# Optimization experiments

Measured on AMD Instinct MI355X. Metric: run time of the kernel, lower is better.

The kernel has to match this reference:

```python
import jax, jax.numpy as jnp
import numpy as np

N, T, E, A, D, O, S, R = 64, 1000, 512, 256, 256, 80, 64, 2
ATT_RANGE = 10
H = 4 * D  # LSTM hidden size = 1024
K = 31     # location conv kernel width


def setup_inputs() -> dict:
    key = jax.random.key(0)
    ks = jax.random.split(key, 16)
    def rn(k, shape, scale=0.05):
        return (jax.random.normal(k, shape) * scale).astype(jnp.float32)
    return {
        "input_enc": jax.random.normal(ks[0], (N, T, E), jnp.float32),
        "input_dec": jax.random.normal(ks[1], (N, O), jnp.float32),
        "spkr_vec": jax.random.normal(ks[2], (N, 1, S), jnp.float32),
        "lengths_enc": jnp.full((N,), T, dtype=jnp.int32),
        "w_enc": rn(ks[3], (E, A)), "b_enc": jnp.zeros((A,), jnp.float32),
        "w_spkr": rn(ks[4], (S, A)),
        "conv_w": rn(ks[5], (A, 1, K)),
        "w_proj": rn(ks[6], (A, 1)), "b_proj": jnp.zeros((1,), jnp.float32),
        "w_p1": rn(ks[7], (O + S, 2 * D)), "b_p1": jnp.zeros((2 * D,), jnp.float32),
        "w_p2": rn(ks[8], (2 * D, D)), "b_p2": jnp.zeros((D,), jnp.float32),
        "w_ih0": rn(ks[9], (E + D + S, 4 * H)), "w_hh0": rn(ks[10], (H, 4 * H)),
        "b_ih0": jnp.zeros((4 * H,), jnp.float32), "b_hh0": jnp.zeros((4 * H,), jnp.float32),
        "w_ih1": rn(ks[11], (H, 4 * H)), "w_hh1": rn(ks[12], (H, 4 * H)),
        "b_ih1": jnp.zeros((4 * H,), jnp.float32), "b_hh1": jnp.zeros((4 * H,), jnp.float32),
        "w_out": rn(ks[13], (E + H, O * R)), "b_out": jnp.zeros((O * R,), jnp.float32),
    }


def _softsign(x):
    return x / (1.0 + jnp.abs(x))


def _lstm_cell_zero_state(x, w_ih, b_ih, b_hh):
    # h0 = c0 = 0, so the w_hh contribution vanishes on the first step
    gates = x @ w_ih + b_ih + b_hh          # [N, 4H]
    i, f, g, o = jnp.split(gates, 4, axis=-1)  # torch gate order i,f,g,o
    c = jax.nn.sigmoid(i) * jnp.tanh(g)
    return jax.nn.sigmoid(o) * jnp.tanh(c)


def reference(input_enc, input_dec, spkr_vec, lengths_enc,
              w_enc, b_enc, w_spkr, conv_w, w_proj, b_proj,
              w_p1, b_p1, w_p2, b_p2,
              w_ih0, w_hh0, b_ih0, b_hh0, w_ih1, w_hh1, b_ih1, b_hh1,
              w_out, b_out):
    n, t_enc, _ = input_enc.shape
    # initial attention weights: one-hot at t=0 (null_state branch)
    a0 = jnp.zeros((n, t_enc), input_enc.dtype).at[:, 0].set(1.0)

    bias_enc = _softsign(input_enc @ w_enc + b_enc)   # [N, T, A]
    bias_spkr = _softsign(spkr_vec @ w_spkr)          # [N, 1, A] broadcast

    # location features: conv1d over prev attention, padding 15, no bias
    prev_feat = jax.lax.conv_general_dilated(
        a0[:, None, :], conv_w, (1,), [(K // 2, K // 2)],
        dimension_numbers=("NCH", "OIH", "NCH"))    # [N, A, T]
    prev_feat = prev_feat.transpose(0, 2, 1)          # [N, T, A]

    # hidden is None on the first step -> in_att_dec = 0
    e = bias_enc + bias_spkr + prev_feat              # [N, T, A]

    # windowed attention mask around argmax of previous weights (no grad)
    max_idx = jnp.argmax(a0, axis=1)                  # [N]
    lim = jnp.maximum(lengths_enc.astype(jnp.int32) - 1, 0)  # [N]
    offs = jnp.arange(ATT_RANGE, dtype=jnp.int32)
    idx1 = jnp.minimum(jnp.maximum(max_idx[:, None] + offs, 0), lim[:, None])
    idx2 = jnp.minimum(jnp.maximum(max_idx[:, None] - offs, 0), lim[:, None])
    idxs = jnp.concatenate([idx1, idx2], axis=1)      # [N, 2*ATT_RANGE]
    rows = jnp.arange(n)[:, None]
    att_mask = jnp.zeros((n, t_enc), e.dtype).at[rows, idxs].set(1.0)
    att_mask = jax.lax.stop_gradient(att_mask)

    logit = (jnp.tanh(e) @ w_proj + b_proj)[..., 0]   # [N, T]
    logit = logit - jnp.max(logit, axis=1, keepdims=True)
    w = jnp.exp(logit) * att_mask
    att = w / jnp.maximum(jnp.sum(w, axis=1, keepdims=True), 1e-12)  # F.normalize p=1

    context = jnp.einsum("nt,nte->ne", att, input_enc)  # [N, E]

    # prenet (dropout in eval mode = identity)
    spkr = spkr_vec[:, 0, :]
    pre = jnp.concatenate([input_dec, spkr], axis=-1)
    pre = jax.nn.relu(pre @ w_p1 + b_p1)
    pre = jax.nn.relu(pre @ w_p2 + b_p2)               # [N, D]

    x = jnp.concatenate([pre, context, spkr], axis=-1)  # [N, D+E+S]
    h1 = _lstm_cell_zero_state(x, w_ih0, b_ih0, b_hh0)   # [N, H]
    h2 = _lstm_cell_zero_state(h1, w_ih1, b_ih1, b_hh1)  # [N, H]
    _ = (w_hh0, w_hh1)  # recurrent weights unused on first step (zero state)

    dec = jnp.concatenate([h2, context], axis=-1)        # [N, H+E]
    out = (dec @ w_out + b_out).reshape(n, R, O)         # [N, r_factor, O]
    return out
```

## Files before the change

kernel.cpp:

```cpp
#include <hip/hip_runtime.h>
#include <hip/hip_bf16.h>
#include <math.h>

#define N_   64
#define T_   1000
#define E_   512
#define A_   256
#define O_   80
#define S_   64
#define H_   1024
#define G4_  4096
#define KC_  31

__device__ __forceinline__ float sigmoidf_(float x) { return 1.f / (1.f + __expf(-x)); }
__device__ __forceinline__ float softsignf_(float x) { return x / (1.f + fabsf(x)); }

__global__ __launch_bounds__(512) void logits_kernel(
    const float* __restrict__ enc,
    const float* __restrict__ spkr,
    const float* __restrict__ w_enc,
    const float* __restrict__ b_enc,
    const float* __restrict__ w_spkr,
    const float* __restrict__ conv_w,
    const float* __restrict__ w_proj,
    float* __restrict__ part) {
  int n  = blockIdx.x;
  int aq = blockIdx.y;
  int tid = threadIdx.x;
  int al = tid & 63;
  int kw = tid >> 6;
  int a  = aq * 64 + al;

  __shared__ float smem[5120];
  __shared__ float sp[S_];
  __shared__ float bsl[S_];

  if (tid < S_) sp[tid] = spkr[n * S_ + tid];
  {
    const float4* src = (const float4*)(enc + (size_t)n * T_ * E_);
    float4* dst = (float4*)smem;
    for (int i = tid; i < 1280; i += 512) dst[i] = src[i];
  }
  __syncthreads();

  if (tid < S_) {
    float b = 0.f;
    #pragma unroll 8
    for (int s = 0; s < S_; ++s) b += sp[s] * w_spkr[s * A_ + aq * 64 + tid];
    bsl[tid] = softsignf_(b);
  }

  float acc[10];
  #pragma unroll
  for (int t = 0; t < 10; ++t) acc[t] = 0.f;
  const int kbase = kw * 64;
  const float* wcol = w_enc + a;
  #pragma unroll 8
  for (int k = 0; k < 64; ++k) {
    float we = wcol[(size_t)(kbase + k) * A_];
    #pragma unroll
    for (int t = 0; t < 10; ++t)
      acc[t] = fmaf(smem[t * E_ + kbase + k], we, acc[t]);
  }

  __syncthreads();
  #pragma unroll
  for (int t = 0; t < 10; ++t) smem[(kw * 10 + t) * 64 + al] = acc[t];
  __syncthreads();

  #pragma unroll
  for (int tb = 0; tb < 10; tb += 8) {
    int t = tb + kw;
    if (t < 10 && (tb == 0 || kw < 2)) {
      float p = b_enc[a];
      #pragma unroll
      for (int w = 0; w < 8; ++w) p += smem[(w * 10 + t) * 64 + al];
      float e = softsignf_(p) + bsl[al] + conv_w[a * KC_ + (15 - t)];
      float l = tanhf(e) * w_proj[a];
      #pragma unroll
      for (int off = 32; off > 0; off >>= 1) l += __shfl_down(l, off);
      if (al == 0) part[(n * 10 + t) * 4 + aq] = l;
    }
  }
}

__global__ __launch_bounds__(512) void ctx_prenet_kernel(
    const float* __restrict__ enc,
    const float* __restrict__ dec_in,
    const float* __restrict__ spkr,
    const int*   __restrict__ lengths,
    const float* __restrict__ part,
    const float* __restrict__ w_p1,
    const float* __restrict__ b_p1,
    const float* __restrict__ w_p2,
    const float* __restrict__ b_p2,
    float* __restrict__ xbuf) {
  int n = blockIdx.x;
  int tid = threadIdx.x;
  __shared__ float att[10];
  __shared__ float incat[O_ + S_];
  __shared__ float pre1[512];
  __shared__ float pp2[2][A_];

  if (tid < S_) {
    float s = spkr[n * S_ + tid];
    incat[O_ + tid] = s;
    xbuf[n * 832 + 768 + tid] = s;
  }
  if (tid < O_) incat[tid] = dec_in[n * O_ + tid];
  if (tid == 0) {
    int lim = lengths[n] - 1; if (lim < 0) lim = 0;
    int tmax = lim < 9 ? lim : 9;
    float lg[10];
    float m = -1e30f;
    for (int t = 0; t <= tmax; ++t) {
      const float* p = &part[(n * 10 + t) * 4];
      lg[t] = p[0] + p[1] + p[2] + p[3];
      m = fmaxf(m, lg[t]);
    }
    float ssum = 0.f;
    for (int t = 0; t <= tmax; ++t) { float w = __expf(lg[t] - m); att[t] = w; ssum += w; }
    float inv = 1.f / fmaxf(ssum, 1e-12f);
    for (int t = 0; t <= tmax; ++t) att[t] *= inv;
    for (int t = tmax + 1; t < 10; ++t) att[t] = 0.f;
  }
  __syncthreads();

  {
    float c = 0.f;
    #pragma unroll
    for (int t = 0; t < 10; ++t)
      c = fmaf(att[t], enc[(size_t)n * T_ * E_ + t * E_ + tid], c);
    xbuf[n * 832 + 256 + tid] = c;
  }

  {
    float v = b_p1[tid];
    #pragma unroll 8
    for (int k = 0; k < O_ + S_; ++k) v = fmaf(incat[k], w_p1[k * 512 + tid], v);
    pre1[tid] = fmaxf(v, 0.f);
  }
  __syncthreads();

  {
    int c  = tid & 255;
    int kh = tid >> 8;
    float v = 0.f;
    #pragma unroll 8
    for (int k = kh * 256; k < kh * 256 + 256; ++k)
      v = fmaf(pre1[k], w_p2[k * A_ + c], v);
    pp2[kh][c] = v;
  }
  __syncthreads();
  if (tid < A_) {
    float v = b_p2[tid] + pp2[0][tid] + pp2[1][tid];
    xbuf[n * 832 + tid] = fmaxf(v, 0.f);
  }
}

__global__ __launch_bounds__(512) void gemm_gates_kernel(
    const float* __restrict__ X, int ldx, int K,
    const float* __restrict__ W,
    const float* __restrict__ b1,
    const float* __restrict__ b2,
    float* __restrict__ G) {
  int bt = blockIdx.x;
  int c0 = bt * 16; if (c0 >= 1024) c0 += 1024;
  int tid = threadIdx.x;
  int kh  = tid >> 8;
  int lt  = tid & 255;
  int tr  = lt >> 4;
  int tc  = lt & 15;
  int c   = c0 + tc;
  int Kh  = K >> 1;
  int kbeg = kh * Kh;
  int NC  = Kh >> 5;

  int rr  = lt & 63;
  int kb8 = (lt >> 6) << 3;
  int wr  = lt >> 4;
  int wc  = lt & 15;

  __shared__ float xs[2][2][32][64];
  __shared__ float wsl[2][2][32][16];
  __shared__ float red[16][16][4];

  const float* xsrc = X + (size_t)rr * ldx + kbeg + kb8;
  const float* wsrc = W + (size_t)(kbeg + wr) * G4_ + c0 + wc;

  float4 xv0 = ((const float4*)xsrc)[0];
  float4 xv1 = ((const float4*)(xsrc + 4))[0];
  float  wv0 = wsrc[0];
  float  wv1 = wsrc[(size_t)16 * G4_];
  {
    float* d = &xs[kh][0][kb8][rr];
    d[0]   = xv0.x; d[64]  = xv0.y; d[128] = xv0.z; d[192] = xv0.w;
    d[256] = xv1.x; d[320] = xv1.y; d[384] = xv1.z; d[448] = xv1.w;
    wsl[kh][0][wr][wc]      = wv0;
    wsl[kh][0][wr + 16][wc] = wv1;
  }
  __syncthreads();

  float acc0 = 0.f, acc1 = 0.f, acc2 = 0.f, acc3 = 0.f;
  for (int ch = 0; ch < NC; ++ch) {
    int buf = ch & 1;
    bool more = (ch + 1 < NC);
    if (more) {
      const float* s = xsrc + (ch + 1) * 32;
      xv0 = ((const float4*)s)[0];
      xv1 = ((const float4*)(s + 4))[0];
      const float* wsp = wsrc + (size_t)(ch + 1) * 32 * G4_;
      wv0 = wsp[0];
      wv1 = wsp[(size_t)16 * G4_];
    }
    const float* xb = &xs[kh][buf][0][tr * 4];
    const float* wb = &wsl[kh][buf][0][tc];
    #pragma unroll
    for (int kk = 0; kk < 32; ++kk) {
      float w = wb[kk * 16];
      float4 xv = *(const float4*)(xb + kk * 64);
      acc0 = fmaf(xv.x, w, acc0);
      acc1 = fmaf(xv.y, w, acc1);
      acc2 = fmaf(xv.z, w, acc2);
      acc3 = fmaf(xv.w, w, acc3);
    }
    if (more) {
      float* d = &xs[kh][buf ^ 1][kb8][rr];
      d[0]   = xv0.x; d[64]  = xv0.y; d[128] = xv0.z; d[192] = xv0.w;
      d[256] = xv1.x; d[320] = xv1.y; d[384] = xv1.z; d[448] = xv1.w;
      wsl[kh][buf ^ 1][wr][wc]      = wv0;
      wsl[kh][buf ^ 1][wr + 16][wc] = wv1;
    }
    __syncthreads();
  }

  if (kh == 1) {
    red[tr][tc][0] = acc0; red[tr][tc][1] = acc1;
    red[tr][tc][2] = acc2; red[tr][tc][3] = acc3;
  }
  __syncthreads();
  if (kh == 0) {
    float bb = b1[c] + b2[c];
    int r = tr * 4;
    G[(size_t)(r + 0) * G4_ + c] = acc0 + red[tr][tc][0] + bb;
    G[(size_t)(r + 1) * G4_ + c] = acc1 + red[tr][tc][1] + bb;
    G[(size_t)(r + 2) * G4_ + c] = acc2 + red[tr][tc][2] + bb;
    G[(size_t)(r + 3) * G4_ + c] = acc3 + red[tr][tc][3] + bb;
  }
}

__global__ void lstm_act_kernel(const float* __restrict__ G, float* __restrict__ H) {
  int idx = blockIdx.x * 256 + threadIdx.x;
  int n = idx >> 10;
  int j = idx & 1023;
  float gi = G[(size_t)n * G4_ + j];
  float gg = G[(size_t)n * G4_ + 2048 + j];
  float go = G[(size_t)n * G4_ + 3072 + j];
  float cc = sigmoidf_(gi) * tanhf(gg);
  H[n * H_ + j] = sigmoidf_(go) * tanhf(cc);
}

#define DLP 1544
__global__ __launch_bounds__(512) void out_kernel(
    const float* __restrict__ gates,
    const float* __restrict__ xbuf,
    const float* __restrict__ w_out,
    const float* __restrict__ b_out,
    float* __restrict__ out) {
  int bn = blockIdx.x >> 3;
  int c0 = (blockIdx.x & 7) * 20;
  int tid = threadIdx.x;
  __shared__ float dl[8][DLP];
  __shared__ float pp[3][160];

  for (int idx = tid; idx < 8 * 1536; idx += 512) {
    int nl = idx / 1536;
    int k  = idx % 1536;
    int n  = bn * 8 + nl;
    if (k < 1024) {
      float gi = gates[(size_t)n * G4_ + k];
      float gg = gates[(size_t)n * G4_ + 2048 + k];
      float go = gates[(size_t)n * G4_ + 3072 + k];
      dl[nl][k] = sigmoidf_(go) * tanhf(sigmoidf_(gi) * tanhf(gg));
    } else {
      dl[nl][k] = xbuf[n * 832 + 256 + (k - 1024)];
    }
  }
  __syncthreads();

  if (tid < 480) {
    int kq = tid / 160;
    int o  = tid % 160;
    int nl = o / 20;
    int cl = o % 20;
    const float* wp = w_out + (size_t)(kq * 512) * 160 + c0 + cl;
    const float* dp = &dl[nl][kq * 512];
    float acc = 0.f;
    #pragma unroll 8
    for (int k = 0; k < 512; ++k) acc = fmaf(dp[k], wp[(size_t)k * 160], acc);
    pp[kq][o] = acc;
  }
  __syncthreads();
  if (tid < 160) {
    int nl = tid / 20;
    int cl = tid % 20;
    float v = b_out[c0 + cl] + pp[0][tid] + pp[1][tid] + pp[2][tid];
    out[(size_t)(bn * 8 + nl) * 160 + c0 + cl] = v;
  }
}

extern "C" void kernel_launch(void* const* d_in, const int* in_sizes, int n_in,
                              void* d_out, int out_size, void* d_ws, size_t ws_size,
                              hipStream_t stream) {
  const float* input_enc = (const float*)d_in[0];
  const float* input_dec = (const float*)d_in[1];
  const float* spkr_vec  = (const float*)d_in[2];
  const int*   lengths   = (const int*)  d_in[3];
  const float* w_enc     = (const float*)d_in[4];
  const float* b_enc     = (const float*)d_in[5];
  const float* w_spkr    = (const float*)d_in[6];
  const float* conv_w    = (const float*)d_in[7];
  const float* w_proj    = (const float*)d_in[8];
  const float* w_p1      = (const float*)d_in[10];
  const float* b_p1      = (const float*)d_in[11];
  const float* w_p2      = (const float*)d_in[12];
  const float* b_p2      = (const float*)d_in[13];
  const float* w_ih0     = (const float*)d_in[14];
  const float* b_ih0     = (const float*)d_in[16];
  const float* b_hh0     = (const float*)d_in[17];
  const float* w_ih1     = (const float*)d_in[18];
  const float* b_ih1     = (const float*)d_in[20];
  const float* b_hh1     = (const float*)d_in[21];
  const float* w_out     = (const float*)d_in[22];
  const float* b_out     = (const float*)d_in[23];

  float* ws    = (float*)d_ws;
  float* part  = ws;
  float* xbuf  = ws + 4096;
  float* gates = ws + 65536;
  float* h1    = ws + 327680;
  float* out   = (float*)d_out;

  hipLaunchKernelGGL(logits_kernel, dim3(64, 4), dim3(512), 0, stream,
                     input_enc, spkr_vec, w_enc, b_enc, w_spkr, conv_w, w_proj, part);
  hipLaunchKernelGGL(ctx_prenet_kernel, dim3(64), dim3(512), 0, stream,
                     input_enc, input_dec, spkr_vec, lengths, part,
                     w_p1, b_p1, w_p2, b_p2, xbuf);
  hipLaunchKernelGGL(gemm_gates_kernel, dim3(192), dim3(512), 0, stream,
                     xbuf, 832, 832, w_ih0, b_ih0, b_hh0, gates);
  hipLaunchKernelGGL(lstm_act_kernel, dim3(256), dim3(256), 0, stream, gates, h1);
  hipLaunchKernelGGL(gemm_gates_kernel, dim3(192), dim3(512), 0, stream,
                     h1, 1024, 1024, w_ih1, b_ih1, b_hh1, gates);
  hipLaunchKernelGGL(out_kernel, dim3(64), dim3(512), 0, stream,
                     gates, xbuf, w_out, b_out, out);
}
```

Measured before the change: 106.0 us.

## Fuse attention logits with context/prenet kernel and load GEMM weights directly into registers

Merges the logits kernel and the context/prenet kernel into one 1024-thread block per batch row. The fused block keeps the encoder frames in LDS and reduces partial logits on chip, which removes one launch and the global partial buffer. The gates GEMM now loads each thread's 32 weight values per chunk straight from global memory into registers instead of staging them through shared memory. The trade-offs are lower grid parallelism in the fused kernel (64 blocks instead of 256), higher register pressure, and weight loads that are no longer prefetched across chunks.

```diff
diff --git a/kernel.cpp b/kernel.cpp
--- a/kernel.cpp
+++ b/kernel.cpp
@@ -15,145 +15,136 @@
 __device__ __forceinline__ float sigmoidf_(float x) { return 1.f / (1.f + __expf(-x)); }
 __device__ __forceinline__ float softsignf_(float x) { return x / (1.f + fabsf(x)); }
 
-__global__ __launch_bounds__(512) void logits_kernel(
+__global__ __launch_bounds__(1024) void att_prenet_kernel(
     const float* __restrict__ enc,
+    const float* __restrict__ dec_in,
     const float* __restrict__ spkr,
+    const int*   __restrict__ lengths,
     const float* __restrict__ w_enc,
     const float* __restrict__ b_enc,
     const float* __restrict__ w_spkr,
     const float* __restrict__ conv_w,
     const float* __restrict__ w_proj,
-    float* __restrict__ part) {
-  int n  = blockIdx.x;
-  int aq = blockIdx.y;
-  int tid = threadIdx.x;
-  int al = tid & 63;
-  int kw = tid >> 6;
-  int a  = aq * 64 + al;
-
-  __shared__ float smem[5120];
-  __shared__ float sp[S_];
-  __shared__ float bsl[S_];
-
-  if (tid < S_) sp[tid] = spkr[n * S_ + tid];
-  {
-    const float4* src = (const float4*)(enc + (size_t)n * T_ * E_);
-    float4* dst = (float4*)smem;
-    for (int i = tid; i < 1280; i += 512) dst[i] = src[i];
-  }
-  __syncthreads();
-
-  if (tid < S_) {
-    float b = 0.f;
-    #pragma unroll 8
-    for (int s = 0; s < S_; ++s) b += sp[s] * w_spkr[s * A_ + aq * 64 + tid];
-    bsl[tid] = softsignf_(b);
-  }
-
-  float acc[10];
-  #pragma unroll
-  for (int t = 0; t < 10; ++t) acc[t] = 0.f;
-  const int kbase = kw * 64;
-  const float* wcol = w_enc + a;
-  #pragma unroll 8
-  for (int k = 0; k < 64; ++k) {
-    float we = wcol[(size_t)(kbase + k) * A_];
-    #pragma unroll
-    for (int t = 0; t < 10; ++t)
-      acc[t] = fmaf(smem[t * E_ + kbase + k], we, acc[t]);
-  }
-
-  __syncthreads();
-  #pragma unroll
-  for (int t = 0; t < 10; ++t) smem[(kw * 10 + t) * 64 + al] = acc[t];
-  __syncthreads();
-
-  #pragma unroll
-  for (int tb = 0; tb < 10; tb += 8) {
-    int t = tb + kw;
-    if (t < 10 && (tb == 0 || kw < 2)) {
-      float p = b_enc[a];
-      #pragma unroll
-      for (int w = 0; w < 8; ++w) p += smem[(w * 10 + t) * 64 + al];
-      float e = softsignf_(p) + bsl[al] + conv_w[a * KC_ + (15 - t)];
-      float l = tanhf(e) * w_proj[a];
-      #pragma unroll
-      for (int off = 32; off > 0; off >>= 1) l += __shfl_down(l, off);
-      if (al == 0) part[(n * 10 + t) * 4 + aq] = l;
-    }
-  }
-}
-
-__global__ __launch_bounds__(512) void ctx_prenet_kernel(
-    const float* __restrict__ enc,
-    const float* __restrict__ dec_in,
-    const float* __restrict__ spkr,
-    const int*   __restrict__ lengths,
-    const float* __restrict__ part,
     const float* __restrict__ w_p1,
     const float* __restrict__ b_p1,
     const float* __restrict__ w_p2,
     const float* __restrict__ b_p2,
     float* __restrict__ xbuf) {
-  int n = blockIdx.x;
-  int tid = threadIdx.x;
+  int n    = blockIdx.x;
+  int tid  = threadIdx.x;
+  int lane = tid & 63;
+  int w    = tid >> 6;
+  int aq   = w >> 2;
+  int kw   = w & 3;
+  int a    = aq * 64 + lane;
+
+  __shared__ float er[5120];
+  __shared__ float plds[10240];
+  __shared__ float sp[S_];
+  __shared__ float bsl[A_];
   __shared__ float att[10];
-  __shared__ float incat[O_ + S_];
-  __shared__ float pre1[512];
-  __shared__ float pp2[2][A_];
-
-  if (tid < S_) {
-    float s = spkr[n * S_ + tid];
-    incat[O_ + tid] = s;
-    xbuf[n * 832 + 768 + tid] = s;
-  }
+  __shared__ float incat[144];
+  __shared__ float lgred[10][4];
+
+  if (tid < S_) sp[tid] = spkr[n * S_ + tid];
   if (tid < O_) incat[tid] = dec_in[n * O_ + tid];
+  else if (tid < 144) incat[tid] = spkr[n * S_ + tid - O_];
+  {
+    const float4* src = (const float4*)(enc + (size_t)n * T_ * E_);
+    float4* dst = (float4*)er;
+    for (int i = tid; i < 1280; i += 1024) dst[i] = src[i];
+  }
+  __syncthreads();
+
+  if (tid < A_) {
+    float b = 0.f;
+    #pragma unroll 8
+    for (int s = 0; s < S_; ++s) b = fmaf(sp[s], w_spkr[s * A_ + tid], b);
+    bsl[tid] = softsignf_(b);
+  }
+
+  float acc[10];
+  #pragma unroll
+  for (int t = 0; t < 10; ++t) acc[t] = 0.f;
+  const int kbase = kw * 128;
+  const float* wcol = w_enc + a;
+  #pragma unroll 8
+  for (int k = 0; k < 128; ++k) {
+    float we = wcol[(size_t)(kbase + k) * A_];
+    #pragma unroll
+    for (int t = 0; t < 10; ++t)
+      acc[t] = fmaf(er[t * E_ + kbase + k], we, acc[t]);
+  }
+  #pragma unroll
+  for (int t = 0; t < 10; ++t) plds[w * 640 + t * 64 + lane] = acc[t];
+  __syncthreads();
+
+  #pragma unroll
+  for (int it = 0; it < 3; ++it) {
+    int idx = tid + it * 1024;
+    if (idx < 2560) {
+      int t   = idx >> 8;
+      int aa  = idx & 255;
+      int aaq = aa >> 6;
+      int al  = aa & 63;
+      float p = plds[(aaq * 4 + 0) * 640 + t * 64 + al]
+              + plds[(aaq * 4 + 1) * 640 + t * 64 + al]
+              + plds[(aaq * 4 + 2) * 640 + t * 64 + al]
+              + plds[(aaq * 4 + 3) * 640 + t * 64 + al];
+      float e = softsignf_(p + b_enc[aa]) + bsl[aa] + conv_w[aa * KC_ + (15 - t)];
+      float l = tanhf(e) * w_proj[aa];
+      #pragma unroll
+      for (int off = 32; off > 0; off >>= 1) l += __shfl_down(l, off);
+      if (al == 0) lgred[t][aaq] = l;
+    }
+  }
+  __syncthreads();
+
   if (tid == 0) {
     int lim = lengths[n] - 1; if (lim < 0) lim = 0;
     int tmax = lim < 9 ? lim : 9;
     float lg[10];
     float m = -1e30f;
     for (int t = 0; t <= tmax; ++t) {
-      const float* p = &part[(n * 10 + t) * 4];
-      lg[t] = p[0] + p[1] + p[2] + p[3];
+      lg[t] = lgred[t][0] + lgred[t][1] + lgred[t][2] + lgred[t][3];
       m = fmaxf(m, lg[t]);
     }
     float ssum = 0.f;
-    for (int t = 0; t <= tmax; ++t) { float w = __expf(lg[t] - m); att[t] = w; ssum += w; }
+    for (int t = 0; t <= tmax; ++t) { float x = __expf(lg[t] - m); att[t] = x; ssum += x; }
     float inv = 1.f / fmaxf(ssum, 1e-12f);
     for (int t = 0; t <= tmax; ++t) att[t] *= inv;
     for (int t = tmax + 1; t < 10; ++t) att[t] = 0.f;
   }
   __syncthreads();
 
-  {
+  if (tid < 512) {
     float c = 0.f;
     #pragma unroll
-    for (int t = 0; t < 10; ++t)
-      c = fmaf(att[t], enc[(size_t)n * T_ * E_ + t * E_ + tid], c);
+    for (int t = 0; t < 10; ++t) c = fmaf(att[t], er[t * E_ + tid], c);
     xbuf[n * 832 + 256 + tid] = c;
-  }
-
-  {
-    float v = b_p1[tid];
+    if (tid < S_) xbuf[n * 832 + 768 + tid] = sp[tid];
+  } else {
+    int c = tid - 512;
+    float v = b_p1[c];
     #pragma unroll 8
-    for (int k = 0; k < O_ + S_; ++k) v = fmaf(incat[k], w_p1[k * 512 + tid], v);
-    pre1[tid] = fmaxf(v, 0.f);
+    for (int k = 0; k < 144; ++k) v = fmaf(incat[k], w_p1[k * 512 + c], v);
+    plds[c] = fmaxf(v, 0.f);
   }
   __syncthreads();
 
   {
     int c  = tid & 255;
-    int kh = tid >> 8;
+    int kq = tid >> 8;
     float v = 0.f;
     #pragma unroll 8
-    for (int k = kh * 256; k < kh * 256 + 256; ++k)
-      v = fmaf(pre1[k], w_p2[k * A_ + c], v);
-    pp2[kh][c] = v;
+    for (int k = kq * 128; k < kq * 128 + 128; ++k)
+      v = fmaf(plds[k], w_p2[k * A_ + c], v);
+    plds[1024 + kq * 256 + c] = v;
   }
   __syncthreads();
   if (tid < A_) {
-    float v = b_p2[tid] + pp2[0][tid] + pp2[1][tid];
+    float v = b_p2[tid] + plds[1024 + tid] + plds[1280 + tid]
+            + plds[1536 + tid] + plds[1792 + tid];
     xbuf[n * 832 + tid] = fmaxf(v, 0.f);
   }
 }
@@ -178,58 +169,47 @@
 
   int rr  = lt & 63;
   int kb8 = (lt >> 6) << 3;
-  int wr  = lt >> 4;
-  int wc  = lt & 15;
 
   __shared__ float xs[2][2][32][64];
-  __shared__ float wsl[2][2][32][16];
   __shared__ float red[16][16][4];
 
   const float* xsrc = X + (size_t)rr * ldx + kbeg + kb8;
-  const float* wsrc = W + (size_t)(kbeg + wr) * G4_ + c0 + wc;
 
   float4 xv0 = ((const float4*)xsrc)[0];
   float4 xv1 = ((const float4*)(xsrc + 4))[0];
-  float  wv0 = wsrc[0];
-  float  wv1 = wsrc[(size_t)16 * G4_];
   {
     float* d = &xs[kh][0][kb8][rr];
     d[0]   = xv0.x; d[64]  = xv0.y; d[128] = xv0.z; d[192] = xv0.w;
     d[256] = xv1.x; d[320] = xv1.y; d[384] = xv1.z; d[448] = xv1.w;
-    wsl[kh][0][wr][wc]      = wv0;
-    wsl[kh][0][wr + 16][wc] = wv1;
   }
   __syncthreads();
 
   float acc0 = 0.f, acc1 = 0.f, acc2 = 0.f, acc3 = 0.f;
   for (int ch = 0; ch < NC; ++ch) {
     int buf = ch & 1;
+    float wreg[32];
+    const float* wp = W + (size_t)(kbeg + ch * 32) * G4_ + c;
+    #pragma unroll
+    for (int kk = 0; kk < 32; ++kk) wreg[kk] = wp[(size_t)kk * G4_];
     bool more = (ch + 1 < NC);
     if (more) {
       const float* s = xsrc + (ch + 1) * 32;
       xv0 = ((const float4*)s)[0];
       xv1 = ((const float4*)(s + 4))[0];
-      const float* wsp = wsrc + (size_t)(ch + 1) * 32 * G4_;
-      wv0 = wsp[0];
-      wv1 = wsp[(size_t)16 * G4_];
     }
     const float* xb = &xs[kh][buf][0][tr * 4];
-    const float* wb = &wsl[kh][buf][0][tc];
     #pragma unroll
     for (int kk = 0; kk < 32; ++kk) {
-      float w = wb[kk * 16];
       float4 xv = *(const float4*)(xb + kk * 64);
-      acc0 = fmaf(xv.x, w, acc0);
-      acc1 = fmaf(xv.y, w, acc1);
-      acc2 = fmaf(xv.z, w, acc2);
-      acc3 = fmaf(xv.w, w, acc3);
+      acc0 = fmaf(xv.x, wreg[kk], acc0);
+      acc1 = fmaf(xv.y, wreg[kk], acc1);
+      acc2 = fmaf(xv.z, wreg[kk], acc2);
+      acc3 = fmaf(xv.w, wreg[kk], acc3);
     }
     if (more) {
       float* d = &xs[kh][buf ^ 1][kb8][rr];
       d[0]   = xv0.x; d[64]  = xv0.y; d[128] = xv0.z; d[192] = xv0.w;
       d[256] = xv1.x; d[320] = xv1.y; d[384] = xv1.z; d[448] = xv1.w;
-      wsl[kh][buf ^ 1][wr][wc]      = wv0;
-      wsl[kh][buf ^ 1][wr + 16][wc] = wv1;
     }
     __syncthreads();
   }
@@ -335,16 +315,14 @@
   const float* b_out     = (const float*)d_in[23];
 
   float* ws    = (float*)d_ws;
-  float* part  = ws;
   float* xbuf  = ws + 4096;
   float* gates = ws + 65536;
   float* h1    = ws + 327680;
   float* out   = (float*)d_out;
 
-  hipLaunchKernelGGL(logits_kernel, dim3(64, 4), dim3(512), 0, stream,
-                     input_enc, spkr_vec, w_enc, b_enc, w_spkr, conv_w, w_proj, part);
-  hipLaunchKernelGGL(ctx_prenet_kernel, dim3(64), dim3(512), 0, stream,
-                     input_enc, input_dec, spkr_vec, lengths, part,
+  hipLaunchKernelGGL(att_prenet_kernel, dim3(64), dim3(1024), 0, stream,
+                     input_enc, input_dec, spkr_vec, lengths,
+                     w_enc, b_enc, w_spkr, conv_w, w_proj,
                      w_p1, b_p1, w_p2, b_p2, xbuf);
   hipLaunchKernelGGL(gemm_gates_kernel, dim3(192), dim3(512), 0, stream,
                      xbuf, 832, 832, w_ih0, b_ih0, b_hh0, gates);
```

Measured after the change: 118.2 us. +11.5%, slower.
